# Kernel optimization log

Hardware: AMD Instinct MI355X
Metric: run time of the kernel (lower is better)

Reference implementation:

```python
import jax, jax.numpy as jnp
import numpy as np

N9, N10, F = 6000, 9000, 128
ALPHA = 0.2  # LeakyReLU negative slope
NEG_INF = -9e15


def setup_inputs() -> dict:
    key = jax.random.key(0)
    k1, k2, k3, k4, k5 = jax.random.split(key, 5)
    U_9 = jax.random.normal(k1, (N9, F), dtype=jnp.float32) * 0.03
    U_10 = jax.random.normal(k2, (N10, F), dtype=jnp.float32) * 0.03
    # xavier_uniform with gain=1.414 for a: limit = gain*sqrt(6/(fan_in+fan_out))
    lim = 1.414 * np.sqrt(6.0 / (2 * F + 1))
    a = jax.random.uniform(k3, (2 * F, 1), dtype=jnp.float32, minval=-lim, maxval=lim)
    # sparse 0/1 code-mapping adjacencies, avg degree ~4
    adj_9to10 = (jax.random.uniform(k4, (N9, N10)) < 4.0 / N10).astype(jnp.float32)
    adj_10to9 = (jax.random.uniform(k5, (N10, N9)) < 4.0 / N9).astype(jnp.float32)
    return {"version": 0, "U_9": U_9, "U_10": U_10, "a": a,
            "adj_9to10": adj_9to10, "adj_10to9": adj_10to9}


def _gat(query, key_feat, adj, a):
    # a splits into the query-half and key-half of the attention vector
    Fd = query.shape[1]
    a1 = a[:Fd, 0]   # [F]
    a2 = a[Fd:, 0]   # [F]
    qa1 = query @ a1        # [Nq]
    qa2 = query @ a2        # [Nq]
    ka2 = key_feat @ a2     # [Nk]
    # self column: leakyrelu([q, q] @ a)
    self_e = jax.nn.leaky_relu(qa1 + qa2, ALPHA)                 # [Nq]
    # cross scores at edge positions: leakyrelu(q_i.a1 + k_j.a2);
    # non-edge entries differ from the torch sparse->dense zeros but are
    # masked to -9e15 below, so the output math is identical.
    e_cross = jax.nn.leaky_relu(qa1[:, None] + ka2[None, :], ALPHA)  # [Nq, Nk]
    ones_col = jnp.ones((query.shape[0], 1), dtype=adj.dtype)
    adj_full = jnp.concatenate([ones_col, adj], axis=1)          # [Nq, Nk+1]
    scores = jnp.concatenate([self_e[:, None], e_cross], axis=1)  # [Nq, Nk+1]
    scores = jnp.where(adj_full > 0, scores, NEG_INF)
    attn = jax.nn.softmax(scores, axis=-1) * adj_full
    attn = jnp.where(jnp.isnan(attn), 0.0, attn)
    h_prime = attn[:, :1] * query + attn[:, 1:] @ key_feat       # [Nq, F]
    return jax.nn.elu(h_prime)


def reference(version, U_9, U_10, a, adj_9to10, adj_10to9):
    if version == 0:  # 'mimiciv_icd9'
        return _gat(U_9, U_10, adj_9to10, a)
    else:
        return _gat(U_10, U_9, adj_10to9, a)
```

## Files before the change

kernel.cpp:

```cpp
#include <hip/hip_runtime.h>
#include <math.h>

#define N9   6000
#define N10  9000
#define FDIM 128
#define ALPHA 0.2f
#define MAXNBR 128
#define ROWBLOCKS 2048

__global__ __launch_bounds__(64)
void gat_dots_kernel(const int* __restrict__ version,
                     const float* __restrict__ U9,
                     const float* __restrict__ U10,
                     const float* __restrict__ a,
                     float* __restrict__ qa1,
                     float* __restrict__ qa2,
                     float* __restrict__ ka2) {
    const int v  = version[0];
    const int nq = v ? N10 : N9;
    const int nk = v ? N9  : N10;
    const float* __restrict__ Q = v ? U10 : U9;
    const float* __restrict__ K = v ? U9  : U10;
    const float* __restrict__ a1 = a;
    const float* __restrict__ a2 = a + FDIM;

    const int row  = blockIdx.x;
    const int lane = threadIdx.x;

    if (row < nq) {
        const float* x = Q + (size_t)row * FDIM;
        float x0 = x[lane], x1 = x[lane + 64];
        float s1 = x0 * a1[lane] + x1 * a1[lane + 64];
        float s2 = x0 * a2[lane] + x1 * a2[lane + 64];
        #pragma unroll
        for (int o = 32; o > 0; o >>= 1) {
            s1 += __shfl_down(s1, o);
            s2 += __shfl_down(s2, o);
        }
        if (lane == 0) { qa1[row] = s1; qa2[row] = s2; }
    } else {
        const int r = row - nq;
        if (r < nk) {
            const float* x = K + (size_t)r * FDIM;
            float s2 = x[lane] * a2[lane] + x[lane + 64] * a2[lane + 64];
            #pragma unroll
            for (int o = 32; o > 0; o >>= 1) s2 += __shfl_down(s2, o);
            if (lane == 0) ka2[r] = s2;
        }
    }
}

__global__ __launch_bounds__(256)
void gat_row_kernel(const int* __restrict__ version,
                    const float* __restrict__ U9,
                    const float* __restrict__ U10,
                    const float* __restrict__ adj9to10,
                    const float* __restrict__ adj10to9,
                    const float* __restrict__ qa1,
                    const float* __restrict__ qa2,
                    const float* __restrict__ ka2,
                    float* __restrict__ out) {
    const int v  = version[0];
    const int nq = v ? N10 : N9;
    const int nk = v ? N9  : N10;

    const float* __restrict__ Q      = v ? U10 : U9;
    const float* __restrict__ K      = v ? U9  : U10;
    const float* __restrict__ adjmat = v ? adj10to9 : adj9to10;

    __shared__ int   s_cnt;
    __shared__ float s_wself;
    __shared__ int   s_j[MAXNBR];
    __shared__ float s_e[MAXNBR];
    __shared__ float s_w[MAXNBR];

    const int t  = threadIdx.x;
    const int n4 = nk >> 2;

    for (int i = blockIdx.x; i < nq; i += gridDim.x) {
        if (t == 0) s_cnt = 0;
        __syncthreads();

        const float qa1i = qa1[i];
        const float4* __restrict__ adj4 = (const float4*)(adjmat + (size_t)i * nk);

        for (int p0 = t; p0 < n4; p0 += 256 * 4) {
            const int p1 = p0 + 256, p2 = p0 + 512, p3 = p0 + 768;
            float4 r0 = adj4[p0];
            float4 r1 = make_float4(0.f, 0.f, 0.f, 0.f);
            float4 r2 = r1, r3 = r1;
            if (p1 < n4) r1 = adj4[p1];
            if (p2 < n4) r2 = adj4[p2];
            if (p3 < n4) r3 = adj4[p3];

            float4 rr[4] = {r0, r1, r2, r3};
            int    pp[4] = {p0, p1, p2, p3};
            #pragma unroll
            for (int u = 0; u < 4; ++u) {
                float4 vv = rr[u];
                if (vv.x > 0.f || vv.y > 0.f || vv.z > 0.f || vv.w > 0.f) {
                    float va[4] = {vv.x, vv.y, vv.z, vv.w};
                    #pragma unroll
                    for (int c = 0; c < 4; ++c) {
                        if (va[c] > 0.f) {
                            int idx = atomicAdd(&s_cnt, 1);
                            if (idx < MAXNBR) {
                                int j = pp[u] * 4 + c;
                                float e = qa1i + ka2[j];
                                e = (e >= 0.f) ? e : ALPHA * e;
                                s_j[idx] = j;
                                s_e[idx] = e;
                            }
                        }
                    }
                }
            }
        }
        __syncthreads();

        const int cnt = (s_cnt < MAXNBR) ? s_cnt : MAXNBR;

        if (t == 0) {
            float se = qa1i + qa2[i];
            se = (se >= 0.f) ? se : ALPHA * se;
            float m = se;
            for (int c = 0; c < cnt; ++c) m = fmaxf(m, s_e[c]);
            float wself = expf(se - m);
            float wsum  = wself;
            for (int c = 0; c < cnt; ++c) {
                float w = expf(s_e[c] - m);
                s_w[c] = w;
                wsum += w;
            }
            float inv = 1.f / wsum;
            s_wself = wself * inv;
            for (int c = 0; c < cnt; ++c) s_w[c] *= inv;
        }
        __syncthreads();

        if (t < FDIM) {
            float h = s_wself * Q[(size_t)i * FDIM + t];
            for (int c = 0; c < cnt; ++c) {
                h += s_w[c] * K[(size_t)s_j[c] * FDIM + t];
            }
            h = (h > 0.f) ? h : expm1f(h);
            out[(size_t)i * FDIM + t] = h;
        }
        __syncthreads();
    }
}

extern "C" void kernel_launch(void* const* d_in, const int* in_sizes, int n_in,
                              void* d_out, int out_size, void* d_ws, size_t ws_size,
                              hipStream_t stream) {
    const int*   d_version = (const int*)d_in[0];
    const float* d_U9      = (const float*)d_in[1];
    const float* d_U10     = (const float*)d_in[2];
    const float* d_a       = (const float*)d_in[3];
    const float* d_adj9    = (const float*)d_in[4];
    const float* d_adj10   = (const float*)d_in[5];
    float*       d_o       = (float*)d_out;

    float* w_qa1 = (float*)d_ws;
    float* w_qa2 = w_qa1 + N10;
    float* w_ka2 = w_qa2 + N10;

    gat_dots_kernel<<<N9 + N10, 64, 0, stream>>>(
        d_version, d_U9, d_U10, d_a, w_qa1, w_qa2, w_ka2);

    gat_row_kernel<<<ROWBLOCKS, 256, 0, stream>>>(
        d_version, d_U9, d_U10, d_adj9, d_adj10,
        w_qa1, w_qa2, w_ka2, d_o);
}
```

Baseline: 48.38 us.

## Fuse projection dot-products into row kernel and stage neighbor rows in LDS

Removes the separate dot-product kernel and computes q·a1, q·a2 and k·a2 only for the rows and neighbors each block actually touches, with neighbor feature rows cached in shared memory for the aggregation. The adjacency scan now uses nontemporal loads. This saves a kernel launch and the full pass over both feature matrices, but adds per-neighbor wave reductions and more LDS use, which may lower occupancy. MAXNBR drops to 64, which assumes no row has more than 64 neighbors.

```diff
diff --git a/kernel.cpp b/kernel.cpp
--- a/kernel.cpp
+++ b/kernel.cpp
@@ -1,116 +1,89 @@
 #include <hip/hip_runtime.h>
 #include <math.h>
 
-#define N9   6000
-#define N10  9000
-#define FDIM 128
-#define ALPHA 0.2f
-#define MAXNBR 128
+#define N9     6000
+#define N10    9000
+#define FDIM   128
+#define ALPHA  0.2f
+#define MAXNBR 64
 #define ROWBLOCKS 2048
 
-__global__ __launch_bounds__(64)
-void gat_dots_kernel(const int* __restrict__ version,
-                     const float* __restrict__ U9,
-                     const float* __restrict__ U10,
-                     const float* __restrict__ a,
-                     float* __restrict__ qa1,
-                     float* __restrict__ qa2,
-                     float* __restrict__ ka2) {
+typedef float f32x4 __attribute__((ext_vector_type(4)));
+
+__global__ __launch_bounds__(256)
+void gat_fused_kernel(const int* __restrict__ version,
+                      const float* __restrict__ U9,
+                      const float* __restrict__ U10,
+                      const float* __restrict__ a,
+                      const float* __restrict__ adj9to10,
+                      const float* __restrict__ adj10to9,
+                      float* __restrict__ out) {
     const int v  = version[0];
     const int nq = v ? N10 : N9;
     const int nk = v ? N9  : N10;
-    const float* __restrict__ Q = v ? U10 : U9;
-    const float* __restrict__ K = v ? U9  : U10;
-    const float* __restrict__ a1 = a;
-    const float* __restrict__ a2 = a + FDIM;
-
-    const int row  = blockIdx.x;
-    const int lane = threadIdx.x;
-
-    if (row < nq) {
-        const float* x = Q + (size_t)row * FDIM;
-        float x0 = x[lane], x1 = x[lane + 64];
-        float s1 = x0 * a1[lane] + x1 * a1[lane + 64];
-        float s2 = x0 * a2[lane] + x1 * a2[lane + 64];
-        #pragma unroll
-        for (int o = 32; o > 0; o >>= 1) {
-            s1 += __shfl_down(s1, o);
-            s2 += __shfl_down(s2, o);
-        }
-        if (lane == 0) { qa1[row] = s1; qa2[row] = s2; }
-    } else {
-        const int r = row - nq;
-        if (r < nk) {
-            const float* x = K + (size_t)r * FDIM;
-            float s2 = x[lane] * a2[lane] + x[lane + 64] * a2[lane + 64];
-            #pragma unroll
-            for (int o = 32; o > 0; o >>= 1) s2 += __shfl_down(s2, o);
-            if (lane == 0) ka2[r] = s2;
-        }
-    }
-}
-
-__global__ __launch_bounds__(256)
-void gat_row_kernel(const int* __restrict__ version,
-                    const float* __restrict__ U9,
-                    const float* __restrict__ U10,
-                    const float* __restrict__ adj9to10,
-                    const float* __restrict__ adj10to9,
-                    const float* __restrict__ qa1,
-                    const float* __restrict__ qa2,
-                    const float* __restrict__ ka2,
-                    float* __restrict__ out) {
-    const int v  = version[0];
-    const int nq = v ? N10 : N9;
-    const int nk = v ? N9  : N10;
-
     const float* __restrict__ Q      = v ? U10 : U9;
     const float* __restrict__ K      = v ? U9  : U10;
     const float* __restrict__ adjmat = v ? adj10to9 : adj9to10;
 
-    __shared__ int   s_cnt;
-    __shared__ float s_wself;
+    __shared__ float s_a1[FDIM];
+    __shared__ float s_a2[FDIM];
+    __shared__ float s_q[FDIM];
+    __shared__ float s_k[MAXNBR][FDIM];
     __shared__ int   s_j[MAXNBR];
     __shared__ float s_e[MAXNBR];
     __shared__ float s_w[MAXNBR];
+    __shared__ int   s_cnt;
+    __shared__ float s_qa1, s_qa2, s_wself;
 
-    const int t  = threadIdx.x;
+    const int t    = threadIdx.x;
+    const int wave = t >> 6;
+    const int lane = t & 63;
+
+    if (t < FDIM) { s_a1[t] = a[t]; s_a2[t] = a[FDIM + t]; }
+    __syncthreads();
+
     const int n4 = nk >> 2;
 
     for (int i = blockIdx.x; i < nq; i += gridDim.x) {
         if (t == 0) s_cnt = 0;
         __syncthreads();
 
-        const float qa1i = qa1[i];
-        const float4* __restrict__ adj4 = (const float4*)(adjmat + (size_t)i * nk);
+        if (wave == 0) {
+            const float* x = Q + (size_t)i * FDIM;
+            float x0 = x[lane], x1 = x[lane + 64];
+            s_q[lane] = x0; s_q[lane + 64] = x1;
+            float s1 = x0 * s_a1[lane] + x1 * s_a1[lane + 64];
+            float s2 = x0 * s_a2[lane] + x1 * s_a2[lane + 64];
+            #pragma unroll
+            for (int o = 32; o > 0; o >>= 1) {
+                s1 += __shfl_down(s1, o);
+                s2 += __shfl_down(s2, o);
+            }
+            if (lane == 0) { s_qa1 = s1; s_qa2 = s2; }
+        }
 
+        const f32x4* __restrict__ adj4 = (const f32x4*)(adjmat + (size_t)i * nk);
         for (int p0 = t; p0 < n4; p0 += 256 * 4) {
             const int p1 = p0 + 256, p2 = p0 + 512, p3 = p0 + 768;
-            float4 r0 = adj4[p0];
-            float4 r1 = make_float4(0.f, 0.f, 0.f, 0.f);
-            float4 r2 = r1, r3 = r1;
-            if (p1 < n4) r1 = adj4[p1];
-            if (p2 < n4) r2 = adj4[p2];
-            if (p3 < n4) r3 = adj4[p3];
+            f32x4 r0 = __builtin_nontemporal_load(&adj4[p0]);
+            f32x4 r1 = (f32x4)(0.f);
+            f32x4 r2 = r1, r3 = r1;
+            if (p1 < n4) r1 = __builtin_nontemporal_load(&adj4[p1]);
+            if (p2 < n4) r2 = __builtin_nontemporal_load(&adj4[p2]);
+            if (p3 < n4) r3 = __builtin_nontemporal_load(&adj4[p3]);
 
-            float4 rr[4] = {r0, r1, r2, r3};
-            int    pp[4] = {p0, p1, p2, p3};
+            f32x4 rr[4] = {r0, r1, r2, r3};
+            int   pp[4] = {p0, p1, p2, p3};
             #pragma unroll
             for (int u = 0; u < 4; ++u) {
-                float4 vv = rr[u];
+                f32x4 vv = rr[u];
                 if (vv.x > 0.f || vv.y > 0.f || vv.z > 0.f || vv.w > 0.f) {
                     float va[4] = {vv.x, vv.y, vv.z, vv.w};
                     #pragma unroll
                     for (int c = 0; c < 4; ++c) {
                         if (va[c] > 0.f) {
                             int idx = atomicAdd(&s_cnt, 1);
-                            if (idx < MAXNBR) {
-                                int j = pp[u] * 4 + c;
-                                float e = qa1i + ka2[j];
-                                e = (e >= 0.f) ? e : ALPHA * e;
-                                s_j[idx] = j;
-                                s_e[idx] = e;
-                            }
+                            if (idx < MAXNBR) s_j[idx] = pp[u] * 4 + c;
                         }
                     }
                 }
@@ -120,8 +93,23 @@
 
         const int cnt = (s_cnt < MAXNBR) ? s_cnt : MAXNBR;
 
+        for (int c = wave; c < cnt; c += 4) {
+            const int j = s_j[c];
+            const float* k = K + (size_t)j * FDIM;
+            float x0 = k[lane], x1 = k[lane + 64];
+            s_k[c][lane] = x0; s_k[c][lane + 64] = x1;
+            float s2 = x0 * s_a2[lane] + x1 * s_a2[lane + 64];
+            #pragma unroll
+            for (int o = 32; o > 0; o >>= 1) s2 += __shfl_down(s2, o);
+            if (lane == 0) {
+                float e = s_qa1 + s2;
+                s_e[c] = (e >= 0.f) ? e : ALPHA * e;
+            }
+        }
+        __syncthreads();
+
         if (t == 0) {
-            float se = qa1i + qa2[i];
+            float se = s_qa1 + s_qa2;
             se = (se >= 0.f) ? se : ALPHA * se;
             float m = se;
             for (int c = 0; c < cnt; ++c) m = fmaxf(m, s_e[c]);
@@ -139,10 +127,8 @@
         __syncthreads();
 
         if (t < FDIM) {
-            float h = s_wself * Q[(size_t)i * FDIM + t];
-            for (int c = 0; c < cnt; ++c) {
-                h += s_w[c] * K[(size_t)s_j[c] * FDIM + t];
-            }
+            float h = s_wself * s_q[t];
+            for (int c = 0; c < cnt; ++c) h += s_w[c] * s_k[c][t];
             h = (h > 0.f) ? h : expm1f(h);
             out[(size_t)i * FDIM + t] = h;
         }
@@ -161,14 +147,6 @@
     const float* d_adj10   = (const float*)d_in[5];
     float*       d_o       = (float*)d_out;
 
-    float* w_qa1 = (float*)d_ws;
-    float* w_qa2 = w_qa1 + N10;
-    float* w_ka2 = w_qa2 + N10;
-
-    gat_dots_kernel<<<N9 + N10, 64, 0, stream>>>(
-        d_version, d_U9, d_U10, d_a, w_qa1, w_qa2, w_ka2);
-
-    gat_row_kernel<<<ROWBLOCKS, 256, 0, stream>>>(
-        d_version, d_U9, d_U10, d_adj9, d_adj10,
-        w_qa1, w_qa2, w_ka2, d_o);
+    gat_fused_kernel<<<ROWBLOCKS, 256, 0, stream>>>(
+        d_version, d_U9, d_U10, d_a, d_adj9, d_adj10, d_o);
 }
```

After: 51.03 us. 1.05x slower.
